# Optimization experiments

Measured on AMD Instinct MI355X. Metric: run time of the kernel, lower is better.

Reference implementation:

```python
import jax, jax.numpy as jnp
import numpy as np

B = 4096
T_STEPS = 2048


def setup_inputs() -> dict:
    key = jax.random.key(0)
    k1, k2, k3 = jax.random.split(key, 3)
    inputs = jax.random.normal(k1, (B, T_STEPS), dtype=jnp.float32)
    # replicate torch init: params = rand(t); params /= sum(|params|); alternate signs
    p = jax.random.uniform(k2, (T_STEPS,), dtype=jnp.float32)
    p = p / jnp.sum(jnp.abs(p))
    sign = jnp.where(jnp.arange(T_STEPS) % 2 == 0, jnp.float32(1.0), jnp.float32(-1.0))
    params = p * sign
    bias = jax.random.normal(k3, (1,), dtype=jnp.float32)
    return {"inputs": inputs, "params": params, "bias": bias}


def reference(inputs, params, bias):
    """AR(t) recurrence: for i in [t, 2t): x_i = sum_j x_{i-1-j} * params[j] + bias.
    inputs: [B, t] seed values; returns the t generated values per row, [B, t].
    """
    t_steps = params.shape[0]
    # torch.dot uses inputs reversed (newest first) against params, so the
    # window kept in oldest->newest order pairs with reversed params.
    p_rev = params[::-1]

    def step(window, _):
        # window: [B, t] last t values, oldest -> newest
        new = window @ p_rev + bias[0]  # [B]
        window = jnp.concatenate([window[:, 1:], new[:, None]], axis=1)
        return window, new

    _, outs = jax.lax.scan(step, inputs, None, length=t_steps)
    return outs.T  # [B, t_steps]
```

## Files before the change

### kernel.cpp

```cpp
#include <hip/hip_runtime.h>
#include <hip/hip_bf16.h>

typedef _Float16 f16;
typedef _Float16 f16x8 __attribute__((ext_vector_type(8)));
typedef float f32x4 __attribute__((ext_vector_type(4)));

constexpr int TS = 2048;
constexpr int BB = 4096;

struct ToepShared { char Xs[16384]; char Ws[8192]; };

struct __align__(16) HShared {
  float rq[2048];
  float h[2048];
  float histp_store[2048];
  float part_buf[4096];
};

template <bool REV>
__device__ void toep_body(ToepShared& lds, int w, const f16* __restrict__ Xg,
                          const char* __restrict__ Wg,
                          const float* __restrict__ biasp, void* __restrict__ Yg) {
  char* Xs = lds.Xs;
  char* Ws = lds.Ws;
  const int tid = threadIdx.x;
  const int lane = tid & 63;
  const int wid = tid >> 6;
  const int wrow = (wid >> 1) * 64;
  const int wcol = (wid & 1) * 32;
  const int px = w & 15;
  const int b0 = (w >> 4) * 128;

  float binit = 0.0f;
  if (REV) binit = biasp[0];

  for (int phase = 0; phase < 2; ++phase) {
    const int mblk = phase ? (31 - px) : px;
    const int m0 = mblk * 64;
    const int k0b = REV ? m0 : 0;
    const int k0e = REV ? TS : (m0 + 64);

    f32x4 acc[4][2];
    #pragma unroll
    for (int i = 0; i < 4; ++i)
      #pragma unroll
      for (int j = 0; j < 2; ++j) acc[i][j] = {binit, binit, binit, binit};

    for (int k0 = k0b; k0 < k0e; k0 += 64) {
      __syncthreads();
      #pragma unroll
      for (int t2 = 0; t2 < 4; ++t2) {
        const int t = wid * 4 + t2;
        const int row = t * 8 + (lane >> 3);
        const char* src = (const char*)Xg + ((size_t)(b0 + row) * TS + k0) * 2
                          + (((lane & 7) * 16) ^ ((row & 7) << 4));
        __builtin_amdgcn_global_load_lds(
            (const __attribute__((address_space(1))) unsigned int*)src,
            (__attribute__((address_space(3))) unsigned int*)(Xs + t * 1024),
            16, 0, 0);
      }
      const int dlt = (REV ? (k0 - m0) : (m0 - k0)) >> 6;
      const char* wsrc = Wg + (size_t)dlt * 8192;
      #pragma unroll
      for (int p = 0; p < 2; ++p) {
        const int t = wid * 2 + p;
        __builtin_amdgcn_global_load_lds(
            (const __attribute__((address_space(1))) unsigned int*)(wsrc + t * 1024 + lane * 16),
            (__attribute__((address_space(3))) unsigned int*)(Ws + t * 1024),
            16, 0, 0);
      }
      __syncthreads();

      #pragma unroll
      for (int ks = 0; ks < 2; ++ks) {
        const int colb = ks * 64 + ((lane >> 4) * 16);
        f16x8 af[4], bf[2];
        #pragma unroll
        for (int i = 0; i < 4; ++i) {
          const int row = wrow + i * 16 + (lane & 15);
          af[i] = *(const f16x8*)(Xs + row * 128 + (colb ^ ((row & 7) << 4)));
        }
        #pragma unroll
        for (int j = 0; j < 2; ++j) {
          const int n = wcol + j * 16 + (lane & 15);
          bf[j] = *(const f16x8*)(Ws + n * 128 + (colb ^ ((n & 7) << 4)));
        }
        #pragma unroll
        for (int i = 0; i < 4; ++i)
          #pragma unroll
          for (int j = 0; j < 2; ++j)
            acc[i][j] = __builtin_amdgcn_mfma_f32_16x16x32_f16(
                af[i], bf[j], acc[i][j], 0, 0, 0);
      }
    }

    #pragma unroll
    for (int i = 0; i < 4; ++i) {
      #pragma unroll
      for (int j = 0; j < 2; ++j) {
        #pragma unroll
        for (int r = 0; r < 4; ++r) {
          const int row = b0 + wrow + i * 16 + (lane >> 4) * 4 + r;
          const int col = m0 + wcol + j * 16 + (lane & 15);
          if (REV)
            ((f16*)Yg)[(size_t)row * TS + col] = (f16)acc[i][j][r];
          else
            ((float*)Yg)[(size_t)row * TS + col] = acc[i][j][r];
        }
      }
    }
  }
}

__device__ void h_block_body(HShared& S, const float* __restrict__ params,
                             float* __restrict__ h_g) {
  float* rq = S.rq;
  float* h_s = S.h;
  float* histp = S.histp_store + 1024;
  const int tid = threadIdx.x;
  const int lane = tid & 63;
  const int wave = tid >> 6;

  if (tid < 512) {
    f32x4 pv = *(const f32x4*)&params[2044 - 4 * tid];
    f32x4 v = {pv[3], pv[2], pv[1], pv[0]};
    *(f32x4*)&rq[4 * tid] = v;
  }
  if (tid < 256) {
    f32x4 z = {0.0f, 0.0f, 0.0f, 0.0f};
    *(f32x4*)&S.histp_store[4 * tid] = z;
  }
  __syncthreads();

  if (wave == 0) {
    float hv = (lane == 0) ? 1.0f : 0.0f;
    for (int m = 1; m < 32; ++m) {
      float partial = (lane < m) ? hv * rq[2048 - m + lane] : 0.0f;
      #pragma unroll
      for (int off = 32; off; off >>= 1) partial += __shfl_xor(partial, off);
      if (lane == m) hv = partial;
    }
    if (lane < 32) h_s[lane] = hv;
  }
  __syncthreads();

  #pragma unroll 1
  for (int n = 32; n < 1024; n <<= 1) {
    int NC = n >> 8; if (NC < 1) NC = 1;
    int SPLIT = 16 / NC;
    if (SPLIT > (n >> 2)) SPLIT = n >> 2;
    const int part = n / SPLIT;
    const int T = part >> 2;
    const int c = wave % NC;
    const int s = wave / NC;
    const int iB = c * 256 + (lane << 2);
    const int m0 = s * part;
    const bool act = (s < SPLIT) && (iB < n);

    if (act) {
      float a0 = 0.0f, a1 = 0.0f, a2 = 0.0f, a3 = 0.0f;
      const float* wp = &rq[2048 - n - iB + m0];
      f32x4 prev = *(const f32x4*)(wp - 4);
      for (int t = 0; t < T; ++t) {
        const f32x4 lo = prev;
        const f32x4 hi = *(const f32x4*)(wp + 4 * t);
        const f32x4 h4 = *(const f32x4*)&h_s[m0 + 4 * t];
        a0 += h4[0] * hi[0] + h4[1] * hi[1] + h4[2] * hi[2] + h4[3] * hi[3];
        a1 += h4[0] * lo[3] + h4[1] * hi[0] + h4[2] * hi[1] + h4[3] * hi[2];
        a2 += h4[0] * lo[2] + h4[1] * lo[3] + h4[2] * hi[0] + h4[3] * hi[1];
        a3 += h4[0] * lo[1] + h4[1] * lo[2] + h4[2] * lo[3] + h4[3] * hi[0];
        prev = hi;
      }
      f32x4 out = {a0, a1, a2, a3};
      *(f32x4*)&S.part_buf[s * n + iB] = out;
    }
    __syncthreads();
    if (tid < n) {
      float v = 0.0f;
      for (int s2 = 0; s2 < SPLIT; ++s2) v += S.part_buf[s2 * n + tid];
      histp[tid] = v;
    }
    __syncthreads();

    if (act) {
      int wmax = c * 256 + 255; if (wmax > n - 1) wmax = n - 1;
      int T2 = ((wmax - m0) >> 2) + 1;
      if (T2 > T) T2 = T;
      if (T2 < 0) T2 = 0;
      float a0 = 0.0f, a1 = 0.0f, a2 = 0.0f, a3 = 0.0f;
      const float* hp = &histp[iB - m0];
      f32x4 hi = *(const f32x4*)hp;
      for (int t = 0; t < T2; ++t) {
        const f32x4 lo = *(const f32x4*)(hp - 4 - 4 * t);
        const f32x4 h4 = *(const f32x4*)&h_s[m0 + 4 * t];
        a0 += h4[0] * hi[0] + h4[1] * lo[3] + h4[2] * lo[2] + h4[3] * lo[1];
        a1 += h4[0] * hi[1] + h4[1] * hi[0] + h4[2] * lo[3] + h4[3] * lo[2];
        a2 += h4[0] * hi[2] + h4[1] * hi[1] + h4[2] * hi[0] + h4[3] * lo[3];
        a3 += h4[0] * hi[3] + h4[1] * hi[2] + h4[2] * hi[1] + h4[3] * hi[0];
        hi = lo;
      }
      f32x4 out = {a0, a1, a2, a3};
      *(f32x4*)&S.part_buf[s * n + iB] = out;
    }
    __syncthreads();
    if (tid < n) {
      float v = 0.0f;
      for (int s2 = 0; s2 < SPLIT; ++s2) v += S.part_buf[s2 * n + tid];
      h_s[n + tid] = v;
    }
    __syncthreads();
  }

  if (tid < 256) *(f32x4*)&h_g[4 * tid] = *(const f32x4*)&h_s[4 * tid];
}

__global__ __launch_bounds__(256, 1) void h_H1024(
    const float* __restrict__ params, const float* __restrict__ h_g,
    float* __restrict__ hist_g) {
  __shared__ __align__(16) float rq[2048];
  __shared__ __align__(16) float hl[1024];
  __shared__ __align__(16) float part[1024];
  const int tid = threadIdx.x;
  const int lane = tid & 63;
  const int wave = tid >> 6;
  const int B = blockIdx.x;

  for (int c = tid; c < 512; c += 256) {
    f32x4 pv = *(const f32x4*)&params[2044 - 4 * c];
    f32x4 v = {pv[3], pv[2], pv[1], pv[0]};
    *(f32x4*)&rq[4 * c] = v;
  }
  *(f32x4*)&hl[4 * tid] = *(const f32x4*)&h_g[4 * tid];
  __syncthreads();

  const int iB = B * 256 + (lane << 2);
  const int m0 = wave * 256;
  float a0 = 0.0f, a1 = 0.0f, a2 = 0.0f, a3 = 0.0f;
  const float* wp = &rq[1024 - iB + m0];
  f32x4 prev = *(const f32x4*)(wp - 4);
  #pragma unroll 4
  for (int t = 0; t < 64; ++t) {
    const f32x4 lo = prev;
    const f32x4 hi = *(const f32x4*)(wp + 4 * t);
    const f32x4 h4 = *(const f32x4*)&hl[m0 + 4 * t];
    a0 += h4[0] * hi[0] + h4[1] * hi[1] + h4[2] * hi[2] + h4[3] * hi[3];
    a1 += h4[0] * lo[3] + h4[1] * hi[0] + h4[2] * hi[1] + h4[3] * hi[2];
    a2 += h4[0] * lo[2] + h4[1] * lo[3] + h4[2] * hi[0] + h4[3] * hi[1];
    a3 += h4[0] * lo[1] + h4[1] * lo[2] + h4[2] * lo[3] + h4[3] * hi[0];
    prev = hi;
  }
  f32x4 out = {a0, a1, a2, a3};
  *(f32x4*)&part[wave * 256 + (lane << 2)] = out;
  __syncthreads();
  const float v = (part[tid] + part[256 + tid]) + (part[512 + tid] + part[768 + tid]);
  hist_g[B * 256 + tid] = v;
}

__global__ __launch_bounds__(256, 1) void h_S1024(
    const float* __restrict__ hist_g, float* __restrict__ h_g) {
  __shared__ __align__(16) float hps[2048];
  __shared__ __align__(16) float hl[1024];
  __shared__ __align__(16) float part[1024];
  const int tid = threadIdx.x;
  const int lane = tid & 63;
  const int wave = tid >> 6;
  const int B = blockIdx.x;

  {
    f32x4 z = {0.0f, 0.0f, 0.0f, 0.0f};
    *(f32x4*)&hps[4 * tid] = z;
    *(f32x4*)&hps[1024 + 4 * tid] = *(const f32x4*)&hist_g[4 * tid];
    *(f32x4*)&hl[4 * tid] = *(const f32x4*)&h_g[4 * tid];
  }
  __syncthreads();

  float* histp = hps + 1024;
  const int iB = B * 256 + (lane << 2);
  const int m0 = wave * 256;
  const int wmax = B * 256 + 255;
  int T2 = 0;
  if (wmax >= m0) { T2 = ((wmax - m0) >> 2) + 1; if (T2 > 64) T2 = 64; }

  float a0 = 0.0f, a1 = 0.0f, a2 = 0.0f, a3 = 0.0f;
  const float* hp = &histp[iB - m0];
  f32x4 hi = *(const f32x4*)hp;
  #pragma unroll 4
  for (int t = 0; t < T2; ++t) {
    const f32x4 lo = *(const f32x4*)(hp - 4 - 4 * t);
    const f32x4 h4 = *(const f32x4*)&hl[m0 + 4 * t];
    a0 += h4[0] * hi[0] + h4[1] * lo[3] + h4[2] * lo[2] + h4[3] * lo[1];
    a1 += h4[0] * hi[1] + h4[1] * hi[0] + h4[2] * lo[3] + h4[3] * lo[2];
    a2 += h4[0] * hi[2] + h4[1] * hi[1] + h4[2] * hi[0] + h4[3] * lo[3];
    a3 += h4[0] * hi[3] + h4[1] * hi[2] + h4[2] * hi[1] + h4[3] * hi[0];
    hi = lo;
  }
  f32x4 out = {a0, a1, a2, a3};
  *(f32x4*)&part[wave * 256 + (lane << 2)] = out;
  __syncthreads();
  const float v = (part[tid] + part[256 + tid]) + (part[512 + tid] + part[768 + tid]);
  h_g[1024 + B * 256 + tid] = v;
}

__global__ __launch_bounds__(1024, 1) void conv_prep(
    const float* __restrict__ X, f16* __restrict__ Xh,
    const float* __restrict__ params, char* __restrict__ Wg,
    float* __restrict__ h_g) {
  __shared__ HShared S;
  const int b = blockIdx.x;
  const int tid = threadIdx.x;

  if (b == 0) {
    h_block_body(S, params, h_g);
    return;
  }
  if (b <= 8) {
    const int dlt = (b - 1) * 4 + (tid >> 8);
    char* tile = Wg + (size_t)dlt * 8192;
    const int s2 = tid & 255;
    const int n = s2 >> 2, kq = s2 & 3;
    #pragma unroll
    for (int part = 0; part < 2; ++part) {
      const int k8 = kq * 16 + part * 8;
      f16x8 v;
      #pragma unroll
      for (int ii = 0; ii < 8; ++ii) {
        const int k = k8 + ii;
        const int dd = dlt * 64 + k - n;
        v[ii] = ((unsigned)dd < (unsigned)TS) ? (f16)params[2047 - dd] : (f16)0.0f;
      }
      *(f16x8*)(tile + n * 128 + ((2 * k8) ^ ((n & 7) << 4))) = v;
    }
    return;
  }
  const size_t base = ((size_t)(b - 9) * 1024 + tid) * 16;
  const float4 a0 = *(const float4*)&X[base];
  const float4 a1 = *(const float4*)&X[base + 4];
  const float4 a2 = *(const float4*)&X[base + 8];
  const float4 a3 = *(const float4*)&X[base + 12];
  f16x8 v0 = {(f16)a0.x, (f16)a0.y, (f16)a0.z, (f16)a0.w,
              (f16)a1.x, (f16)a1.y, (f16)a1.z, (f16)a1.w};
  f16x8 v1 = {(f16)a2.x, (f16)a2.y, (f16)a2.z, (f16)a2.w,
              (f16)a3.x, (f16)a3.y, (f16)a3.z, (f16)a3.w};
  *(f16x8*)&Xh[base] = v0;
  *(f16x8*)&Xh[base + 8] = v1;
}

__global__ __launch_bounds__(256, 2) void toep_A(
    const f16* __restrict__ Xh, const char* __restrict__ Wg,
    const float* __restrict__ biasp, f16* __restrict__ u,
    const float* __restrict__ h_g, char* __restrict__ WgC) {
  __shared__ ToepShared lds;
  const int b = blockIdx.x;
  if (b >= 512) {
    const int bw = b - 512;
    const int tid = threadIdx.x;
    const int kq = tid >> 6;
    const int n2 = tid & 63;
    for (int dlt = bw * 8; dlt < bw * 8 + 8; ++dlt) {
      char* tile = WgC + (size_t)dlt * 8192;
      #pragma unroll
      for (int part = 0; part < 2; ++part) {
        const int k8 = kq * 16 + part * 8;
        f16x8 v;
        #pragma unroll
        for (int ii = 0; ii < 8; ++ii) {
          const int dd = dlt * 64 + n2 - (k8 + ii);
          v[ii] = ((unsigned)dd < (unsigned)TS) ? (f16)h_g[dd] : (f16)0.0f;
        }
        *(f16x8*)(tile + n2 * 128 + ((2 * k8) ^ ((n2 & 7) << 4))) = v;
      }
    }
    return;
  }
  toep_body<true>(lds, (b & 7) * 64 + (b >> 3), Xh, Wg, biasp, (void*)u);
}

__global__ __launch_bounds__(256, 2) void toep_C(
    const f16* __restrict__ u, const char* __restrict__ WgC,
    float* __restrict__ out) {
  __shared__ ToepShared lds;
  const int b = blockIdx.x;
  toep_body<false>(lds, (b & 7) * 64 + (b >> 3), u, WgC, nullptr, (void*)out);
}

extern "C" void kernel_launch(void* const* d_in, const int* in_sizes, int n_in,
                              void* d_out, int out_size, void* d_ws, size_t ws_size,
                              hipStream_t stream) {
  const float* inputs = (const float*)d_in[0];
  const float* params = (const float*)d_in[1];
  const float* bias   = (const float*)d_in[2];
  float* out = (float*)d_out;

  char* ws = (char*)d_ws;
  f16*   Xh    = (f16*)ws;
  f16*   u     = (f16*)(ws + (size_t)BB * TS * 2);
  char*  Wg    = ws + (size_t)BB * TS * 4;
  float* h_g   = (float*)(Wg + 64 * 8192);
  float* hist_g = h_g + 2048;

  conv_prep<<<521, 1024, 0, stream>>>(inputs, Xh, params, Wg, h_g);
  h_H1024<<<4, 256, 0, stream>>>(params, h_g, hist_g);
  h_S1024<<<4, 256, 0, stream>>>(hist_g, h_g);
  toep_A<<<516, 256, 0, stream>>>(Xh, Wg, bias, u, h_g, Wg + 32 * 8192);
  toep_C<<<512, 256, 0, stream>>>(u, Wg + 32 * 8192, out);
}
```

Before: 95.50 us.

## Move n=512 impulse-response doubling step from single block to multi-block kernels

The single-block impulse-response doubling loop inside conv_prep now stops at n=256. The n=512 step moves into the generalized h_Hn/h_Sn kernels, which now take n as a parameter and run on 2 blocks, spreading that step's work across more CUs. The partial-sum reductions in the block loop are also vectorized to f32x4. This adds two extra kernel launches in exchange for a shorter serial critical path in block 0 of conv_prep.

Result: slower. 101.5 us (+6.3%).

```diff
diff --git a/kernel.cpp b/kernel.cpp
--- a/kernel.cpp
+++ b/kernel.cpp
@@ -145,15 +145,13 @@
   __syncthreads();
 
   #pragma unroll 1
-  for (int n = 32; n < 1024; n <<= 1) {
-    int NC = n >> 8; if (NC < 1) NC = 1;
-    int SPLIT = 16 / NC;
+  for (int n = 32; n < 512; n <<= 1) {
+    int SPLIT = 16;
     if (SPLIT > (n >> 2)) SPLIT = n >> 2;
     const int part = n / SPLIT;
     const int T = part >> 2;
-    const int c = wave % NC;
-    const int s = wave / NC;
-    const int iB = c * 256 + (lane << 2);
+    const int s = wave;
+    const int iB = lane << 2;
     const int m0 = s * part;
     const bool act = (s < SPLIT) && (iB < n);
 
@@ -175,15 +173,16 @@
       *(f32x4*)&S.part_buf[s * n + iB] = out;
     }
     __syncthreads();
-    if (tid < n) {
-      float v = 0.0f;
-      for (int s2 = 0; s2 < SPLIT; ++s2) v += S.part_buf[s2 * n + tid];
-      histp[tid] = v;
+    if (tid < (n >> 2)) {
+      f32x4 v = {0.0f, 0.0f, 0.0f, 0.0f};
+      for (int s2 = 0; s2 < SPLIT; ++s2)
+        v += *(const f32x4*)&S.part_buf[s2 * n + 4 * tid];
+      *(f32x4*)&histp[4 * tid] = v;
     }
     __syncthreads();
 
     if (act) {
-      int wmax = c * 256 + 255; if (wmax > n - 1) wmax = n - 1;
+      int wmax = n - 1;
       int T2 = ((wmax - m0) >> 2) + 1;
       if (T2 > T) T2 = T;
       if (T2 < 0) T2 = 0;
@@ -203,20 +202,21 @@
       *(f32x4*)&S.part_buf[s * n + iB] = out;
     }
     __syncthreads();
-    if (tid < n) {
-      float v = 0.0f;
-      for (int s2 = 0; s2 < SPLIT; ++s2) v += S.part_buf[s2 * n + tid];
-      h_s[n + tid] = v;
+    if (tid < (n >> 2)) {
+      f32x4 v = {0.0f, 0.0f, 0.0f, 0.0f};
+      for (int s2 = 0; s2 < SPLIT; ++s2)
+        v += *(const f32x4*)&S.part_buf[s2 * n + 4 * tid];
+      *(f32x4*)&h_s[n + 4 * tid] = v;
     }
     __syncthreads();
   }
 
-  if (tid < 256) *(f32x4*)&h_g[4 * tid] = *(const f32x4*)&h_s[4 * tid];
-}
-
-__global__ __launch_bounds__(256, 1) void h_H1024(
+  if (tid < 128) *(f32x4*)&h_g[4 * tid] = *(const f32x4*)&h_s[4 * tid];
+}
+
+__global__ __launch_bounds__(256, 1) void h_Hn(
     const float* __restrict__ params, const float* __restrict__ h_g,
-    float* __restrict__ hist_g) {
+    float* __restrict__ hist_g, int n) {
   __shared__ __align__(16) float rq[2048];
   __shared__ __align__(16) float hl[1024];
   __shared__ __align__(16) float part[1024];
@@ -230,16 +230,19 @@
     f32x4 v = {pv[3], pv[2], pv[1], pv[0]};
     *(f32x4*)&rq[4 * c] = v;
   }
-  *(f32x4*)&hl[4 * tid] = *(const f32x4*)&h_g[4 * tid];
-  __syncthreads();
-
+  for (int c = tid; c < (n >> 2); c += 256)
+    *(f32x4*)&hl[4 * c] = *(const f32x4*)&h_g[4 * c];
+  __syncthreads();
+
+  const int mlen = n >> 2;
+  const int T = mlen >> 2;
   const int iB = B * 256 + (lane << 2);
-  const int m0 = wave * 256;
+  const int m0 = wave * mlen;
   float a0 = 0.0f, a1 = 0.0f, a2 = 0.0f, a3 = 0.0f;
-  const float* wp = &rq[1024 - iB + m0];
+  const float* wp = &rq[2048 - n - iB + m0];
   f32x4 prev = *(const f32x4*)(wp - 4);
   #pragma unroll 4
-  for (int t = 0; t < 64; ++t) {
+  for (int t = 0; t < T; ++t) {
     const f32x4 lo = prev;
     const f32x4 hi = *(const f32x4*)(wp + 4 * t);
     const f32x4 h4 = *(const f32x4*)&hl[m0 + 4 * t];
@@ -256,8 +259,8 @@
   hist_g[B * 256 + tid] = v;
 }
 
-__global__ __launch_bounds__(256, 1) void h_S1024(
-    const float* __restrict__ hist_g, float* __restrict__ h_g) {
+__global__ __launch_bounds__(256, 1) void h_Sn(
+    const float* __restrict__ hist_g, float* __restrict__ h_g, int n) {
   __shared__ __align__(16) float hps[2048];
   __shared__ __align__(16) float hl[1024];
   __shared__ __align__(16) float part[1024];
@@ -269,17 +272,21 @@
   {
     f32x4 z = {0.0f, 0.0f, 0.0f, 0.0f};
     *(f32x4*)&hps[4 * tid] = z;
-    *(f32x4*)&hps[1024 + 4 * tid] = *(const f32x4*)&hist_g[4 * tid];
-    *(f32x4*)&hl[4 * tid] = *(const f32x4*)&h_g[4 * tid];
+  }
+  for (int c = tid; c < (n >> 2); c += 256) {
+    *(f32x4*)&hps[1024 + 4 * c] = *(const f32x4*)&hist_g[4 * c];
+    *(f32x4*)&hl[4 * c] = *(const f32x4*)&h_g[4 * c];
   }
   __syncthreads();
 
   float* histp = hps + 1024;
+  const int mlen = n >> 2;
+  const int Tmax = mlen >> 2;
   const int iB = B * 256 + (lane << 2);
-  const int m0 = wave * 256;
+  const int m0 = wave * mlen;
   const int wmax = B * 256 + 255;
   int T2 = 0;
-  if (wmax >= m0) { T2 = ((wmax - m0) >> 2) + 1; if (T2 > 64) T2 = 64; }
+  if (wmax >= m0) { T2 = ((wmax - m0) >> 2) + 1; if (T2 > Tmax) T2 = Tmax; }
 
   float a0 = 0.0f, a1 = 0.0f, a2 = 0.0f, a3 = 0.0f;
   const float* hp = &histp[iB - m0];
@@ -298,7 +305,7 @@
   *(f32x4*)&part[wave * 256 + (lane << 2)] = out;
   __syncthreads();
   const float v = (part[tid] + part[256 + tid]) + (part[512 + tid] + part[768 + tid]);
-  h_g[1024 + B * 256 + tid] = v;
+  h_g[n + B * 256 + tid] = v;
 }
 
 __global__ __launch_bounds__(1024, 1) void conv_prep(
@@ -392,15 +399,17 @@
   float* out = (float*)d_out;
 
   char* ws = (char*)d_ws;
-  f16*   Xh    = (f16*)ws;
-  f16*   u     = (f16*)(ws + (size_t)BB * TS * 2);
-  char*  Wg    = ws + (size_t)BB * TS * 4;
-  float* h_g   = (float*)(Wg + 64 * 8192);
+  f16*   Xh     = (f16*)ws;
+  f16*   u      = (f16*)(ws + (size_t)BB * TS * 2);
+  char*  Wg     = ws + (size_t)BB * TS * 4;
+  float* h_g    = (float*)(Wg + 64 * 8192);
   float* hist_g = h_g + 2048;
 
   conv_prep<<<521, 1024, 0, stream>>>(inputs, Xh, params, Wg, h_g);
-  h_H1024<<<4, 256, 0, stream>>>(params, h_g, hist_g);
-  h_S1024<<<4, 256, 0, stream>>>(hist_g, h_g);
+  h_Hn<<<2, 256, 0, stream>>>(params, h_g, hist_g, 512);
+  h_Sn<<<2, 256, 0, stream>>>(hist_g, h_g, 512);
+  h_Hn<<<4, 256, 0, stream>>>(params, h_g, hist_g, 1024);
+  h_Sn<<<4, 256, 0, stream>>>(hist_g, h_g, 1024);
   toep_A<<<516, 256, 0, stream>>>(Xh, Wg, bias, u, h_g, Wg + 32 * 8192);
   toep_C<<<512, 256, 0, stream>>>(u, Wg + 32 * 8192, out);
 }
```
